# Kernel tuning notes

Hardware: AMD Instinct MI355X
Metric: run time of the kernel (lower is better)

The kernel has to match this reference:

```python
import jax, jax.numpy as jnp
import numpy as np

HEAD = 8

def setup_inputs() -> dict:
    key = jax.random.key(0)
    k1, k2 = jax.random.split(key)
    B, S, D = 4, 2048, 512
    x = jax.random.normal(k1, (B, S, D), dtype=jnp.float32)
    Wq = jax.random.normal(k2, (D, D), dtype=jnp.float32) * (1.0 / np.sqrt(D))
    return {"x": x, "Wq": Wq}


def reference(x, Wq):
    # Faithful to source: Q, K, V all use linear_q (bug preserved).
    B, S, D = x.shape
    hd = D // HEAD
    q = jnp.einsum('bsd,de->bse', x, Wq)
    # Q = K = V = q
    qh = q.reshape(B, S, HEAD, hd).transpose(0, 2, 1, 3)  # [B,H,S,hd]
    # scale by sqrt(head_dim): inputs.shape[-1] inside ScaleDotAttentionLayer
    scores = jnp.einsum('bhqd,bhkd->bhqk', qh, qh) / jnp.sqrt(jnp.float32(hd))
    weights = jax.nn.softmax(scores, axis=-1)
    ctx = jnp.einsum('bhqk,bhkd->bhqd', weights, qh)
    out = ctx.transpose(0, 2, 1, 3).reshape(B, S, D)
    return out
```

## Files before the change

kernel.cpp:

```cpp
#include <hip/hip_runtime.h>
#include <hip/hip_fp16.h>
#include <math.h>

#define SS 2048
#define DD 512
#define NH 8
#define HD 64

typedef __attribute__((ext_vector_type(8))) short frag_ab;
typedef __attribute__((ext_vector_type(4))) float frag_cd;
typedef __attribute__((ext_vector_type(4))) _Float16 frag_b4;

static __device__ inline unsigned int pack_h2(float x, float y) {
    __half2 t = __floats2half2_rn(x, y);
    return *(unsigned int*)&t;
}

__global__ __launch_bounds__(512, 4) void gemm_kernel(const float* __restrict__ x,
                                                      const float* __restrict__ w,
                                                      unsigned short* __restrict__ q) {
    __shared__ __align__(16) unsigned short Ah[2][128 * 72];
    __shared__ __align__(16) unsigned short Bt[2][64 * 72];
    const int tid = threadIdx.x;
    const int lane = tid & 63, wv = tid >> 6;
    const int a = lane & 15, g = lane >> 4;
    const int bm = blockIdx.x, bn = blockIdx.y;
    const int wr = wv >> 1, wc = wv & 1;

    frag_cd acc[2][2] = {};
    const int ar = tid >> 4;
    const int ac = (tid & 15) * 4;
    const int bnw = tid & 63;
    const int bc  = tid >> 6;
    const int bp  = (bc + 2 * (bnw & 7)) & 7;

    float4 av[4];
    float  bw[8];

    auto load_tiles = [&](int k0) {
        #pragma unroll
        for (int i = 0; i < 4; ++i)
            av[i] = *(const float4*)(x + (size_t)(bm * 128 + ar + 32 * i) * 512 + k0 + ac);
        #pragma unroll
        for (int j = 0; j < 8; ++j)
            bw[j] = w[(size_t)(k0 + bc * 8 + j) * 512 + bn * 64 + bnw];
    };
    auto stage_tiles = [&](int buf) {
        #pragma unroll
        for (int i = 0; i < 4; ++i) {
            uint2 hh = { pack_h2(av[i].x, av[i].y), pack_h2(av[i].z, av[i].w) };
            *(uint2*)&Ah[buf][(ar + 32 * i) * 72 + ac] = hh;
        }
        unsigned int tb[4];
        #pragma unroll
        for (int j = 0; j < 4; ++j)
            tb[j] = pack_h2(bw[2 * j], bw[2 * j + 1]);
        *(uint4*)&Bt[buf][bnw * 72 + bp * 8] = *(uint4*)tb;
    };

    load_tiles(0);
    stage_tiles(0);
    load_tiles(64);
    __syncthreads();

    for (int it = 0; it < 8; ++it) {
        const int cur = it & 1;
        if (it < 7) stage_tiles(cur ^ 1);
        if (it < 6) load_tiles((it + 2) * 64);
        #pragma unroll
        for (int kh = 0; kh < 2; ++kh) {
            frag_ab bf[2], af[2];
            #pragma unroll
            for (int nt = 0; nt < 2; ++nt) {
                const int nr = wc * 32 + nt * 16 + a;
                const int pr = ((kh * 4 + g) + 2 * (nr & 7)) & 7;
                bf[nt] = *(const frag_ab*)&Bt[cur][nr * 72 + pr * 8];
            }
            #pragma unroll
            for (int mt = 0; mt < 2; ++mt)
                af[mt] = *(const frag_ab*)&Ah[cur][(wr * 32 + mt * 16 + a) * 72 + kh * 32 + g * 8];
            #pragma unroll
            for (int mt = 0; mt < 2; ++mt)
                #pragma unroll
                for (int nt = 0; nt < 2; ++nt)
                    acc[mt][nt] = __builtin_amdgcn_mfma_f32_16x16x32_f16(af[mt], bf[nt], acc[mt][nt], 0, 0, 0);
        }
        __syncthreads();
    }
    #pragma unroll
    for (int mt = 0; mt < 2; ++mt)
        #pragma unroll
        for (int nt = 0; nt < 2; ++nt)
            #pragma unroll
            for (int r = 0; r < 4; ++r) {
                const int m = bm * 128 + wr * 32 + mt * 16 + g * 4 + r;
                const int n = bn * 64 + wc * 32 + nt * 16 + a;
                __half hv = __float2half_rn(acc[mt][nt][r]);
                q[(size_t)m * 512 + n] = *(unsigned short*)&hv;
            }
}

__global__ __launch_bounds__(512, 4) void attn_kernel(const __half* __restrict__ qg,
                                                      float* __restrict__ out) {
    __shared__ __align__(16) unsigned char LDSB[69632];
    unsigned short* KtB = (unsigned short*)LDSB;
    unsigned short* VtB = (unsigned short*)(LDSB + 36864);

    const int tid = threadIdx.x;
    const int lane = tid & 63, wv = tid >> 6;
    const int a = lane & 15, g = lane >> 4;
    const int qq = wv & 3;
    const int kv = wv >> 2;
    const int bid = blockIdx.x;
    const int qt = bid & 15;
    const int h  = (bid >> 4) & 7;
    const int b  = bid >> 7;

    const unsigned short* qbh = (const unsigned short*)qg + (size_t)b * SS * DD + h * HD;
    const int qrow0 = qt * 128 + qq * 32;

    frag_ab qf[2][2];
    const __half2 qsc = __float2half2_rn(0.18033688011112042f);
    #pragma unroll
    for (int nt = 0; nt < 2; ++nt)
        #pragma unroll
        for (int kh = 0; kh < 2; ++kh) {
            frag_ab t = *(const frag_ab*)(qbh + (size_t)(qrow0 + nt * 16 + a) * DD + kh * 32 + g * 8);
            __half2* phh = (__half2*)&t;
            #pragma unroll
            for (int i = 0; i < 4; ++i) phh[i] = __hmul2(phh[i], qsc);
            qf[nt][kh] = t;
        }

    frag_cd oacc[4][2] = {};
    float lsum[2] = {0.f, 0.f};

    const int t8 = tid & 255;
    const int f0 = (t8 & 31) * 2;
    const int u8 = t8 >> 5;
    const int r0 = u8 * 8;
    const int keybase = (tid >> 8) * 1024;
    unsigned short* KsBase = KtB + (tid >> 8) * 4608;
    unsigned short* VsBase = VtB + (tid >> 8) * 4096;
    const int vsw = (u8 ^ (t8 & 7)) << 3;

    unsigned int d[8];
    #pragma unroll
    for (int k = 0; k < 8; ++k)
        d[k] = *(const unsigned int*)(qbh + (size_t)(keybase + r0 + k) * DD + f0);

    const unsigned short* KcBase = KtB + kv * 4608;
    const unsigned short* VcBase = VtB + kv * 4096;
    const float coff = -11.541560327111707f;
    const int sv = (a >> 1) & 7;

    auto stage_write = [&](int buf) {
        unsigned short* Ksb = KsBase + buf * 9216;
        unsigned short* Vsb = VsBase + buf * 8192;
        #pragma unroll
        for (int k = 0; k < 8; ++k)
            *(unsigned int*)&Ksb[(r0 + k) * 72 + f0] = d[k];
        unsigned int vlo[4], vhi[4];
        #pragma unroll
        for (int j = 0; j < 4; ++j) {
            vlo[j] = (d[2 * j] & 0xFFFFu) | (d[2 * j + 1] << 16);
            vhi[j] = (d[2 * j] >> 16)     | (d[2 * j + 1] & 0xFFFF0000u);
        }
        *(uint4*)&Vsb[f0 * 64 + vsw]       = *(uint4*)vlo;
        *(uint4*)&Vsb[(f0 + 1) * 64 + vsw] = *(uint4*)vhi;
    };

    stage_write(0);
    #pragma unroll
    for (int k = 0; k < 8; ++k)
        d[k] = *(const unsigned int*)(qbh + (size_t)(keybase + 64 + r0 + k) * DD + f0);
    __syncthreads();

    for (int it = 0; it < 16; ++it) {
        const int cur = it & 1;
        if (it < 15) stage_write(cur ^ 1);
        if (it < 14) {
            const int kb = keybase + (it + 2) * 64;
            #pragma unroll
            for (int k = 0; k < 8; ++k)
                d[k] = *(const unsigned int*)(qbh + (size_t)(kb + r0 + k) * DD + f0);
        }
        const unsigned short* Kc = KcBase + cur * 9216;
        const unsigned short* Vc = VcBase + cur * 8192;

        #pragma unroll
        for (int kt = 0; kt < 4; ++kt) {
            const frag_ab ka0 = *(const frag_ab*)&Kc[(kt * 16 + a) * 72 + g * 8];
            const frag_ab ka1 = *(const frag_ab*)&Kc[(kt * 16 + a) * 72 + 32 + g * 8];
            frag_b4 pbk[2];
            #pragma unroll
            for (int nt = 0; nt < 2; ++nt) {
                frag_cd c = {coff, coff, coff, coff};
                c = __builtin_amdgcn_mfma_f32_16x16x32_f16(ka0, qf[nt][0], c, 0, 0, 0);
                c = __builtin_amdgcn_mfma_f32_16x16x32_f16(ka1, qf[nt][1], c, 0, 0, 0);
                const float p0 = __builtin_amdgcn_exp2f(c[0]);
                const float p1 = __builtin_amdgcn_exp2f(c[1]);
                const float p2 = __builtin_amdgcn_exp2f(c[2]);
                const float p3 = __builtin_amdgcn_exp2f(c[3]);
                lsum[nt] += (p0 + p1) + (p2 + p3);
                union { unsigned int u[2]; frag_b4 hh; } pu;
                pu.u[0] = pack_h2(p0, p1);
                pu.u[1] = pack_h2(p2, p3);
                pbk[nt] = pu.hh;
            }
            const int vch = ((2 * kt + (g >> 1)) ^ sv) << 3;
            const int vof = (g & 1) << 2;
            #pragma unroll
            for (int ft = 0; ft < 4; ++ft) {
                const frag_b4 va = *(const frag_b4*)&Vc[(ft * 16 + a) * 64 + vch + vof];
                oacc[ft][0] = __builtin_amdgcn_mfma_f32_16x16x16f16(va, pbk[0], oacc[ft][0], 0, 0, 0);
                oacc[ft][1] = __builtin_amdgcn_mfma_f32_16x16x16f16(va, pbk[1], oacc[ft][1], 0, 0, 0);
            }
        }
        __syncthreads();
    }

    #pragma unroll
    for (int nt = 0; nt < 2; ++nt) {
        lsum[nt] += __shfl_xor(lsum[nt], 16, 64);
        lsum[nt] += __shfl_xor(lsum[nt], 32, 64);
    }
    float* Obuf = (float*)LDSB;
    float* Lbuf = (float*)(LDSB + 33792);
    if (kv == 1) {
        #pragma unroll
        for (int ft = 0; ft < 4; ++ft)
            #pragma unroll
            for (int nt = 0; nt < 2; ++nt)
                #pragma unroll
                for (int r = 0; r < 4; ++r)
                    Obuf[qq * 2112 + (ft * 16 + g * 4 + r) * 33 + nt * 16 + a] = oacc[ft][nt][r];
        if (g == 0)
            #pragma unroll
            for (int nt = 0; nt < 2; ++nt)
                Lbuf[qq * 32 + nt * 16 + a] = lsum[nt];
    }
    __syncthreads();
    if (kv == 0) {
        #pragma unroll
        for (int nt = 0; nt < 2; ++nt) {
            const float inv = 1.f / (lsum[nt] + Lbuf[qq * 32 + nt * 16 + a]);
            float* op = out + ((size_t)b * SS + qrow0 + nt * 16 + a) * DD + h * HD;
            #pragma unroll
            for (int ft = 0; ft < 4; ++ft) {
                const int fb = ft * 16 + g * 4;
                float4 vv = {
                    (oacc[ft][nt][0] + Obuf[qq * 2112 + (fb + 0) * 33 + nt * 16 + a]) * inv,
                    (oacc[ft][nt][1] + Obuf[qq * 2112 + (fb + 1) * 33 + nt * 16 + a]) * inv,
                    (oacc[ft][nt][2] + Obuf[qq * 2112 + (fb + 2) * 33 + nt * 16 + a]) * inv,
                    (oacc[ft][nt][3] + Obuf[qq * 2112 + (fb + 3) * 33 + nt * 16 + a]) * inv };
                *(float4*)(op + fb) = vv;
            }
        }
    }
}

extern "C" void kernel_launch(void* const* d_in, const int* in_sizes, int n_in,
                              void* d_out, int out_size, void* d_ws, size_t ws_size,
                              hipStream_t stream) {
    const float* x  = (const float*)d_in[0];
    const float* wq = (const float*)d_in[1];
    float* out = (float*)d_out;
    unsigned short* q_h = (unsigned short*)d_ws;

    dim3 ggrid(64, 8);
    gemm_kernel<<<ggrid, 512, 0, stream>>>(x, wq, q_h);
    attn_kernel<<<512, 512, 0, stream>>>((const __half*)q_h, out);
}
```

Before: 121.8 us.

## Fuse projection GEMM and attention into one kernel with grid-wide barrier

Merges the Q-projection GEMM and the attention kernel into a single persistent launch of 512 blocks. An atomic counter in workspace acts as a grid-wide barrier between the GEMM phase and the attention phase, and LDS is reused between the two phases. This removes one kernel launch and the gap between the two kernels. The cost is a spin-wait barrier that relies on all 512 blocks being co-resident (4 blocks per CU by launch bounds) and an extra memset launch to reset the counter.

```diff
diff --git a/kernel.cpp b/kernel.cpp
--- a/kernel.cpp
+++ b/kernel.cpp
@@ -14,6 +14,262 @@
 static __device__ inline unsigned int pack_h2(float x, float y) {
     __half2 t = __floats2half2_rn(x, y);
     return *(unsigned int*)&t;
+}
+
+__global__ __launch_bounds__(512, 4) void fused_kernel(const float* __restrict__ x,
+                                                       const float* __restrict__ w,
+                                                       unsigned short* __restrict__ qh,
+                                                       float* __restrict__ out,
+                                                       unsigned int* __restrict__ bar) {
+    __shared__ __align__(16) unsigned char LDSB[69632];
+    const int tid = threadIdx.x;
+    const int lane = tid & 63, wv = tid >> 6;
+    const int a = lane & 15, g = lane >> 4;
+    const int bid = blockIdx.x;
+
+    {
+        unsigned short* Ah = (unsigned short*)LDSB;
+        unsigned short* Bt = (unsigned short*)(LDSB + 36864);
+        const int bm = bid & 63, bn = bid >> 6;
+        const int wr = wv >> 1, wc = wv & 1;
+
+        frag_cd acc[2][2] = {};
+        const int ar = tid >> 4;
+        const int ac = (tid & 15) * 4;
+        const int bnw = tid & 63;
+        const int bc  = tid >> 6;
+        const int bp  = (bc + 2 * (bnw & 7)) & 7;
+
+        float4 av[4];
+        float  bw[8];
+
+        auto load_tiles = [&](int k0) {
+            #pragma unroll
+            for (int i = 0; i < 4; ++i)
+                av[i] = *(const float4*)(x + (size_t)(bm * 128 + ar + 32 * i) * 512 + k0 + ac);
+            #pragma unroll
+            for (int j = 0; j < 8; ++j)
+                bw[j] = w[(size_t)(k0 + bc * 8 + j) * 512 + bn * 64 + bnw];
+        };
+        auto stage_tiles = [&](int buf) {
+            #pragma unroll
+            for (int i = 0; i < 4; ++i) {
+                uint2 hh = { pack_h2(av[i].x, av[i].y), pack_h2(av[i].z, av[i].w) };
+                *(uint2*)&Ah[buf * 9216 + (ar + 32 * i) * 72 + ac] = hh;
+            }
+            unsigned int tb[4];
+            #pragma unroll
+            for (int j = 0; j < 4; ++j)
+                tb[j] = pack_h2(bw[2 * j], bw[2 * j + 1]);
+            *(uint4*)&Bt[buf * 4608 + bnw * 72 + bp * 8] = *(uint4*)tb;
+        };
+
+        load_tiles(0);
+        stage_tiles(0);
+        load_tiles(64);
+        __syncthreads();
+
+        for (int it = 0; it < 8; ++it) {
+            const int cur = it & 1;
+            if (it < 7) stage_tiles(cur ^ 1);
+            if (it < 6) load_tiles((it + 2) * 64);
+            #pragma unroll
+            for (int kh = 0; kh < 2; ++kh) {
+                frag_ab bf[2], af[2];
+                #pragma unroll
+                for (int nt = 0; nt < 2; ++nt) {
+                    const int nr = wc * 32 + nt * 16 + a;
+                    const int pr = ((kh * 4 + g) + 2 * (nr & 7)) & 7;
+                    bf[nt] = *(const frag_ab*)&Bt[cur * 4608 + nr * 72 + pr * 8];
+                }
+                #pragma unroll
+                for (int mt = 0; mt < 2; ++mt)
+                    af[mt] = *(const frag_ab*)&Ah[cur * 9216 + (wr * 32 + mt * 16 + a) * 72 + kh * 32 + g * 8];
+                #pragma unroll
+                for (int mt = 0; mt < 2; ++mt)
+                    #pragma unroll
+                    for (int nt = 0; nt < 2; ++nt)
+                        acc[mt][nt] = __builtin_amdgcn_mfma_f32_16x16x32_f16(af[mt], bf[nt], acc[mt][nt], 0, 0, 0);
+            }
+            __syncthreads();
+        }
+        #pragma unroll
+        for (int mt = 0; mt < 2; ++mt)
+            #pragma unroll
+            for (int nt = 0; nt < 2; ++nt)
+                #pragma unroll
+                for (int r = 0; r < 4; ++r) {
+                    const int m = bm * 128 + wr * 32 + mt * 16 + g * 4 + r;
+                    const int n = bn * 64 + wc * 32 + nt * 16 + a;
+                    __half hv = __float2half_rn(acc[mt][nt][r]);
+                    qh[(size_t)m * 512 + n] = *(unsigned short*)&hv;
+                }
+    }
+
+    __syncthreads();
+    if (tid == 0) {
+        __threadfence();
+        atomicAdd(bar, 1u);
+        while (__hip_atomic_load(bar, __ATOMIC_RELAXED, __HIP_MEMORY_SCOPE_AGENT) < 512u)
+            __builtin_amdgcn_s_sleep(2);
+    }
+    __syncthreads();
+    __threadfence();
+
+    {
+        const __half* qg = (const __half*)qh;
+        unsigned short* KtB = (unsigned short*)LDSB;
+        unsigned short* VtB = (unsigned short*)(LDSB + 36864);
+
+        const int qq = wv & 3;
+        const int kv = wv >> 2;
+        const int qt = bid & 15;
+        const int h  = (bid >> 4) & 7;
+        const int b  = bid >> 7;
+
+        const unsigned short* qbh = (const unsigned short*)qg + (size_t)b * SS * DD + h * HD;
+        const int qrow0 = qt * 128 + qq * 32;
+
+        frag_ab qf[2][2];
+        const __half2 qsc = __float2half2_rn(0.18033688011112042f);
+        #pragma unroll
+        for (int nt = 0; nt < 2; ++nt)
+            #pragma unroll
+            for (int kh = 0; kh < 2; ++kh) {
+                frag_ab t = *(const frag_ab*)(qbh + (size_t)(qrow0 + nt * 16 + a) * DD + kh * 32 + g * 8);
+                __half2* phh = (__half2*)&t;
+                #pragma unroll
+                for (int i = 0; i < 4; ++i) phh[i] = __hmul2(phh[i], qsc);
+                qf[nt][kh] = t;
+            }
+
+        frag_cd oacc[4][2] = {};
+        float lsum[2] = {0.f, 0.f};
+
+        const int t8 = tid & 255;
+        const int f0 = (t8 & 31) * 2;
+        const int u8 = t8 >> 5;
+        const int r0 = u8 * 8;
+        const int keybase = (tid >> 8) * 1024;
+        unsigned short* KsBase = KtB + (tid >> 8) * 4608;
+        unsigned short* VsBase = VtB + (tid >> 8) * 4096;
+        const int vsw = (u8 ^ (t8 & 7)) << 3;
+
+        unsigned int d[8];
+        #pragma unroll
+        for (int k = 0; k < 8; ++k)
+            d[k] = *(const unsigned int*)(qbh + (size_t)(keybase + r0 + k) * DD + f0);
+
+        const unsigned short* KcBase = KtB + kv * 4608;
+        const unsigned short* VcBase = VtB + kv * 4096;
+        const float coff = -11.541560327111707f;
+        const int sv = (a >> 1) & 7;
+
+        auto stage_write = [&](int buf) {
+            unsigned short* Ksb = KsBase + buf * 9216;
+            unsigned short* Vsb = VsBase + buf * 8192;
+            #pragma unroll
+            for (int k = 0; k < 8; ++k)
+                *(unsigned int*)&Ksb[(r0 + k) * 72 + f0] = d[k];
+            unsigned int vlo[4], vhi[4];
+            #pragma unroll
+            for (int j = 0; j < 4; ++j) {
+                vlo[j] = (d[2 * j] & 0xFFFFu) | (d[2 * j + 1] << 16);
+                vhi[j] = (d[2 * j] >> 16)     | (d[2 * j + 1] & 0xFFFF0000u);
+            }
+            *(uint4*)&Vsb[f0 * 64 + vsw]       = *(uint4*)vlo;
+            *(uint4*)&Vsb[(f0 + 1) * 64 + vsw] = *(uint4*)vhi;
+        };
+
+        stage_write(0);
+        #pragma unroll
+        for (int k = 0; k < 8; ++k)
+            d[k] = *(const unsigned int*)(qbh + (size_t)(keybase + 64 + r0 + k) * DD + f0);
+        __syncthreads();
+
+        for (int it = 0; it < 16; ++it) {
+            const int cur = it & 1;
+            if (it < 15) stage_write(cur ^ 1);
+            if (it < 14) {
+                const int kb = keybase + (it + 2) * 64;
+                #pragma unroll
+                for (int k = 0; k < 8; ++k)
+                    d[k] = *(const unsigned int*)(qbh + (size_t)(kb + r0 + k) * DD + f0);
+            }
+            const unsigned short* Kc = KcBase + cur * 9216;
+            const unsigned short* Vc = VcBase + cur * 8192;
+
+            #pragma unroll
+            for (int kt = 0; kt < 4; ++kt) {
+                const frag_ab ka0 = *(const frag_ab*)&Kc[(kt * 16 + a) * 72 + g * 8];
+                const frag_ab ka1 = *(const frag_ab*)&Kc[(kt * 16 + a) * 72 + 32 + g * 8];
+                frag_b4 pbk[2];
+                #pragma unroll
+                for (int nt = 0; nt < 2; ++nt) {
+                    frag_cd c = {coff, coff, coff, coff};
+                    c = __builtin_amdgcn_mfma_f32_16x16x32_f16(ka0, qf[nt][0], c, 0, 0, 0);
+                    c = __builtin_amdgcn_mfma_f32_16x16x32_f16(ka1, qf[nt][1], c, 0, 0, 0);
+                    const float p0 = __builtin_amdgcn_exp2f(c[0]);
+                    const float p1 = __builtin_amdgcn_exp2f(c[1]);
+                    const float p2 = __builtin_amdgcn_exp2f(c[2]);
+                    const float p3 = __builtin_amdgcn_exp2f(c[3]);
+                    lsum[nt] += (p0 + p1) + (p2 + p3);
+                    union { unsigned int u[2]; frag_b4 hh; } pu;
+                    pu.u[0] = pack_h2(p0, p1);
+                    pu.u[1] = pack_h2(p2, p3);
+                    pbk[nt] = pu.hh;
+                }
+                const int vch = ((2 * kt + (g >> 1)) ^ sv) << 3;
+                const int vof = (g & 1) << 2;
+                #pragma unroll
+                for (int ft = 0; ft < 4; ++ft) {
+                    const frag_b4 va = *(const frag_b4*)&Vc[(ft * 16 + a) * 64 + vch + vof];
+                    oacc[ft][0] = __builtin_amdgcn_mfma_f32_16x16x16f16(va, pbk[0], oacc[ft][0], 0, 0, 0);
+                    oacc[ft][1] = __builtin_amdgcn_mfma_f32_16x16x16f16(va, pbk[1], oacc[ft][1], 0, 0, 0);
+                }
+            }
+            __syncthreads();
+        }
+
+        #pragma unroll
+        for (int nt = 0; nt < 2; ++nt) {
+            lsum[nt] += __shfl_xor(lsum[nt], 16, 64);
+            lsum[nt] += __shfl_xor(lsum[nt], 32, 64);
+        }
+        float* Obuf = (float*)LDSB;
+        float* Lbuf = (float*)(LDSB + 33792);
+        if (kv == 1) {
+            #pragma unroll
+            for (int ft = 0; ft < 4; ++ft)
+                #pragma unroll
+                for (int nt = 0; nt < 2; ++nt)
+                    #pragma unroll
+                    for (int r = 0; r < 4; ++r)
+                        Obuf[qq * 2112 + (ft * 16 + g * 4 + r) * 33 + nt * 16 + a] = oacc[ft][nt][r];
+            if (g == 0)
+                #pragma unroll
+                for (int nt = 0; nt < 2; ++nt)
+                    Lbuf[qq * 32 + nt * 16 + a] = lsum[nt];
+        }
+        __syncthreads();
+        if (kv == 0) {
+            #pragma unroll
+            for (int nt = 0; nt < 2; ++nt) {
+                const float inv = 1.f / (lsum[nt] + Lbuf[qq * 32 + nt * 16 + a]);
+                float* op = out + ((size_t)b * SS + qrow0 + nt * 16 + a) * DD + h * HD;
+                #pragma unroll
+                for (int ft = 0; ft < 4; ++ft) {
+                    const int fb = ft * 16 + g * 4;
+                    float4 vv = {
+                        (oacc[ft][nt][0] + Obuf[qq * 2112 + (fb + 0) * 33 + nt * 16 + a]) * inv,
+                        (oacc[ft][nt][1] + Obuf[qq * 2112 + (fb + 1) * 33 + nt * 16 + a]) * inv,
+                        (oacc[ft][nt][2] + Obuf[qq * 2112 + (fb + 2) * 33 + nt * 16 + a]) * inv,
+                        (oacc[ft][nt][3] + Obuf[qq * 2112 + (fb + 3) * 33 + nt * 16 + a]) * inv };
+                    *(float4*)(op + fb) = vv;
+                }
+            }
+        }
+    }
 }
 
 __global__ __launch_bounds__(512, 4) void gemm_kernel(const float* __restrict__ x,
@@ -267,8 +523,15 @@
     const float* wq = (const float*)d_in[1];
     float* out = (float*)d_out;
     unsigned short* q_h = (unsigned short*)d_ws;
-
-    dim3 ggrid(64, 8);
-    gemm_kernel<<<ggrid, 512, 0, stream>>>(x, wq, q_h);
-    attn_kernel<<<512, 512, 0, stream>>>((const __half*)q_h, out);
+    const size_t QH_BYTES = (size_t)4 * SS * DD * sizeof(unsigned short);
+
+    if (ws_size >= QH_BYTES + 64) {
+        unsigned int* bar = (unsigned int*)((char*)d_ws + QH_BYTES);
+        hipMemsetAsync(bar, 0, 4, stream);
+        fused_kernel<<<512, 512, 0, stream>>>(x, wq, q_h, out, bar);
+    } else {
+        dim3 ggrid(64, 8);
+        gemm_kernel<<<ggrid, 512, 0, stream>>>(x, wq, q_h);
+        attn_kernel<<<512, 512, 0, stream>>>((const __half*)q_h, out);
+    }
 }
```

Result: slower. 229.2 us (+88.1%).
